# Performance work log

Measured on AMD Instinct MI355X. Metric: run time of the kernel, lower is better.

Reference implementation:

```python
import jax, jax.numpy as jnp
import numpy as np

D = 1024
H = 16
DK = D // H
EPS = 1e-5


def _layernorm(x, g, b):
    mu = jnp.mean(x, axis=-1, keepdims=True)
    var = jnp.var(x, axis=-1, keepdims=True)
    return (x - mu) * jax.lax.rsqrt(var + EPS) * g + b


def setup_inputs() -> dict:
    key = jax.random.key(0)
    ks = jax.random.split(key, 8)
    N, T = 4, 2048
    # module initializes Wqkv/Wout with torch.randn (std=1); mimic that scale
    x = jax.random.normal(ks[0], (N, T, D), dtype=jnp.float32)
    mask = jnp.zeros((N, 1, 1, T), dtype=jnp.float32)  # additive padding mask
    Wqkv = jax.random.normal(ks[1], (D, 3 * D), dtype=jnp.float32)
    Wout = jax.random.normal(ks[2], (D, D), dtype=jnp.float32)
    ln1_g = jnp.ones((D,), jnp.float32); ln1_b = jnp.zeros((D,), jnp.float32)
    ln2_g = jnp.ones((D,), jnp.float32); ln2_b = jnp.zeros((D,), jnp.float32)
    s1 = (1.0 / np.sqrt(D)); s2 = (1.0 / np.sqrt(4 * D))
    W1 = jax.random.uniform(ks[3], (D, 4 * D), jnp.float32, -s1, s1)
    b1 = jnp.zeros((4 * D,), jnp.float32)
    W2 = jax.random.uniform(ks[4], (4 * D, D), jnp.float32, -s2, s2)
    b2 = jnp.zeros((D,), jnp.float32)
    return dict(x=x, mask=mask, Wqkv=Wqkv, Wout=Wout, ln1_g=ln1_g, ln1_b=ln1_b,
                ln2_g=ln2_g, ln2_b=ln2_b, W1=W1, b1=b1, W2=W2, b2=b2)


def reference(x, mask, Wqkv, Wout, ln1_g, ln1_b, ln2_g, ln2_b, W1, b1, W2, b2):
    N, T, _ = x.shape
    # --- attention sublayer: Residual(PreNorm(MHSA)) ---
    z = _layernorm(x, ln1_g, ln1_b)
    qkv = z @ Wqkv  # [N,T,3D]
    Q, K, V = jnp.split(qkv, 3, axis=-1)
    Q, K, V = [a.reshape(N, T, H, DK).swapaxes(1, 2) for a in (Q, K, V)]  # [N,H,T,dk]
    scores = jnp.einsum('nhtd,nhsd->nhts', Q, K) * (DK ** -0.5) + mask
    attn = jax.nn.softmax(scores, axis=-1)  # dropout in eval mode = identity
    ctx = jnp.einsum('nhts,nhsd->nhtd', attn, V)
    attn_out = ctx.swapaxes(1, 2).reshape(N, T, D) @ Wout
    x = x + attn_out
    # --- FFN sublayer: Residual(PreNorm(FFN)), exact (erf) GELU ---
    z = _layernorm(x, ln2_g, ln2_b)
    h = jax.nn.gelu(z @ W1 + b1, approximate=False)
    x = x + (h @ W2 + b2)
    return x
```

## Files before the change

kernel.cpp:

```cpp
#include <hip/hip_runtime.h>
#include <math.h>

#define DEV __device__ __forceinline__

typedef short bf16x8 __attribute__((ext_vector_type(8)));
typedef float f32x4 __attribute__((ext_vector_type(4)));

DEV float bf2f(short s){
  union{ float f; unsigned u; } v; v.u = ((unsigned)(unsigned short)s) << 16; return v.f;
}
DEV short f2b(float f){
  union{ float f; unsigned u; } v; v.f = f;
  unsigned r = v.u + 0x7fffu + ((v.u >> 16) & 1u);
  return (short)(r >> 16);
}
DEV unsigned pk2(float a, float b){
  return ((unsigned)(unsigned short)f2b(b) << 16) | (unsigned short)f2b(a);
}

DEV void gll16(const void* g, void* l){
  __builtin_amdgcn_global_load_lds((const __attribute__((address_space(1))) void*)g,
                                   (__attribute__((address_space(3))) void*)l, 16, 0, 0);
}

template<bool SPLIT>
__global__ void tsplit_kernel(const float* __restrict__ in, short* __restrict__ hi,
                              short* __restrict__ lo, int R, int C){
  __shared__ float tile[32][33];
  int tc = blockIdx.x*32, tr = blockIdx.y*32;
  int lx = threadIdx.x, ly = threadIdx.y;
  for (int i = 0; i < 32; i += 8)
    tile[ly+i][lx] = in[(size_t)(tr+ly+i)*C + tc+lx];
  __syncthreads();
  for (int i = 0; i < 32; i += 8){
    float v = tile[lx][ly+i];
    size_t o = (size_t)(tc+ly+i)*R + tr+lx;
    short h_ = f2b(v); hi[o] = h_;
    if constexpr (SPLIT) lo[o] = f2b(v - bf2f(h_));
  }
}

template<bool SPLIT>
__global__ void ln_kernel(const float* __restrict__ x, const float* __restrict__ g,
                          const float* __restrict__ bta, short* __restrict__ hi,
                          short* __restrict__ lo){
  int row = blockIdx.x, tid = threadIdx.x;
  const float* xr = x + (size_t)row*1024;
  float v[4], s = 0.f, q = 0.f;
  #pragma unroll
  for (int i = 0; i < 4; i++){ v[i] = xr[tid + i*256]; s += v[i]; q += v[i]*v[i]; }
  #pragma unroll
  for (int m = 1; m < 64; m <<= 1){ s += __shfl_xor(s, m); q += __shfl_xor(q, m); }
  __shared__ float red[8];
  int wave = tid >> 6, lane = tid & 63;
  if (lane == 0){ red[wave] = s; red[4+wave] = q; }
  __syncthreads();
  s = red[0]+red[1]+red[2]+red[3];
  q = red[4]+red[5]+red[6]+red[7];
  float mu = s * (1.f/1024.f);
  float var = q * (1.f/1024.f) - mu*mu;
  float rstd = rsqrtf(var + 1e-5f);
  #pragma unroll
  for (int i = 0; i < 4; i++){
    int d = tid + i*256;
    float z = (v[i]-mu)*rstd*g[d] + bta[d];
    short h_ = f2b(z);
    hi[(size_t)row*1024 + d] = h_;
    if constexpr (SPLIT) lo[(size_t)row*1024 + d] = f2b(z - bf2f(h_));
  }
}

constexpr int BM = 128, BN = 128, BK = 32;

template<int MODE, bool SPLIT>
__global__ __launch_bounds__(256, 2) void gemm_kernel(
    const short* __restrict__ Ahi, const short* __restrict__ Alo,
    const short* __restrict__ Bhi, const short* __restrict__ Blo,
    int M, int N, int K,
    float* __restrict__ outf, short* __restrict__ outb,
    const float* __restrict__ res, const float* __restrict__ bias,
    short* __restrict__ qhi, short* __restrict__ qlo,
    short* __restrict__ khi, short* __restrict__ klo,
    short* __restrict__ vbf)
{
  __shared__ short lds[(SPLIT ? 4 : 2) * BM * BK];
  short* sAhi = lds;
  short* sBhi = lds + BM*BK;
  short* sAlo = lds;
  short* sBlo = lds;
  if constexpr (SPLIT){ sAlo = lds + 2*BM*BK; sBlo = lds + 3*BM*BK; }

  const int tid = threadIdx.x;
  const int wave = tid >> 6, lane = tid & 63;
  const int bm = blockIdx.y * BM, bn = blockIdx.x * BN;
  const int wm = (wave >> 1) * 64, wn = (wave & 1) * 64;

  f32x4 acc[4][4] = {};

  const int srow = lane >> 2;
  const int skq  = (lane & 3) * 8;

  for (int k0 = 0; k0 < K; k0 += BK){
    #pragma unroll
    for (int i = 0; i < 2; i++){
      int seg = wave*2 + i;
      int row = seg*16 + srow;
      gll16(Ahi + (size_t)(bm+row)*K + k0 + skq, sAhi + seg*16*BK);
      gll16(Bhi + (size_t)(bn+row)*K + k0 + skq, sBhi + seg*16*BK);
      if constexpr (SPLIT){
        gll16(Alo + (size_t)(bm+row)*K + k0 + skq, sAlo + seg*16*BK);
        gll16(Blo + (size_t)(bn+row)*K + k0 + skq, sBlo + seg*16*BK);
      }
    }
    __syncthreads();
    bf16x8 ah[4], bh[4], al[4], bl[4];
    #pragma unroll
    for (int i = 0; i < 4; i++){
      int ra = (wm + i*16 + (lane & 15)) * BK + (lane >> 4) * 8;
      int rb = (wn + i*16 + (lane & 15)) * BK + (lane >> 4) * 8;
      ah[i] = *(const bf16x8*)&sAhi[ra];
      bh[i] = *(const bf16x8*)&sBhi[rb];
      if constexpr (SPLIT){
        al[i] = *(const bf16x8*)&sAlo[ra];
        bl[i] = *(const bf16x8*)&sBlo[rb];
      }
    }
    __syncthreads();
    #pragma unroll
    for (int i = 0; i < 4; i++)
      #pragma unroll
      for (int j = 0; j < 4; j++){
        acc[i][j] = __builtin_amdgcn_mfma_f32_16x16x32_bf16(ah[i], bh[j], acc[i][j], 0, 0, 0);
        if constexpr (SPLIT){
          acc[i][j] = __builtin_amdgcn_mfma_f32_16x16x32_bf16(ah[i], bl[j], acc[i][j], 0, 0, 0);
          acc[i][j] = __builtin_amdgcn_mfma_f32_16x16x32_bf16(al[i], bh[j], acc[i][j], 0, 0, 0);
        }
      }
  }

  const int row0 = bm + wm + (lane >> 4) * 4;
  const int col0 = bn + wn + (lane & 15);
  #pragma unroll
  for (int i = 0; i < 4; i++)
    #pragma unroll
    for (int j = 0; j < 4; j++){
      int col = col0 + j*16;
      #pragma unroll
      for (int r = 0; r < 4; r++){
        int row = row0 + i*16 + r;
        float v = acc[i][j][r];
        if constexpr (MODE == 1){
          size_t o = (size_t)row*N + col;
          outf[o] = res[o] + v;
        } else if constexpr (MODE == 2){
          float t = v + bias[col];
          t = 0.5f * t * (1.0f + erff(t * 0.70710678118654752f));
          outb[(size_t)row*N + col] = f2b(t);
        } else if constexpr (MODE == 3){
          size_t o = (size_t)row*N + col;
          outf[o] = res[o] + v + bias[col];
        } else {
          int nb = row >> 11, tt = row & 2047;
          if (col < 1024){
            int h = col >> 6, dk = col & 63;
            size_t o = ((size_t)(nb*16 + h)*2048 + tt)*64 + dk;
            float vq = v * 0.125f;
            short h_ = f2b(vq); qhi[o] = h_; qlo[o] = f2b(vq - bf2f(h_));
          } else if (col < 2048){
            int c = col - 1024, h = c >> 6, dk = c & 63;
            size_t o = ((size_t)(nb*16 + h)*2048 + tt)*64 + dk;
            short h_ = f2b(v); khi[o] = h_; klo[o] = f2b(v - bf2f(h_));
          } else {
            int c = col - 2048, h = c >> 6, dk = c & 63;
            vbf[((size_t)(nb*16 + h)*64 + dk)*2048 + tt] = f2b(v);
          }
        }
      }
    }
}

__global__ __launch_bounds__(256, 2) void attn_kernel(
    const short* __restrict__ qhi, const short* __restrict__ qlo,
    const short* __restrict__ khi, const short* __restrict__ klo,
    const short* __restrict__ vt,  const float* __restrict__ mask,
    short* __restrict__ ctx)
{
  __shared__ short sKh[128*64];
  __shared__ short sKl[128*64];
  __shared__ short sQV[64*128];
  __shared__ short sP[4*16*128];
  short* sQh = sQV;
  short* sQl = sQV + 4096;
  short* sV  = sQV;

  const int tid = threadIdx.x, wave = tid >> 6, lane = tid & 63;
  const int qd = lane >> 4, n16 = lane & 15;
  const int nh = blockIdx.y, nb = nh >> 4, h = nh & 15;
  const int q0 = blockIdx.x * 64;
  const size_t qoff = ((size_t)nh*2048 + q0)*64;
  const int sw = n16 & 7;

  {
    int cg = ((lane & 7) ^ (lane >> 3)) * 8;
    int rowl = lane >> 3;
    #pragma unroll
    for (int i = 0; i < 2; i++){
      int seg = wave*2 + i;
      int row = seg*8 + rowl;
      gll16(qhi + qoff + (size_t)row*64 + cg, sQh + seg*512);
      gll16(qlo + qoff + (size_t)row*64 + cg, sQl + seg*512);
    }
  }
  __syncthreads();

  bf16x8 bqh[2], bql[2];
  #pragma unroll
  for (int k2 = 0; k2 < 2; k2++){
    int off = (wave*16 + n16)*64 + (((k2*4 + qd) ^ sw) << 3);
    bqh[k2] = *(const bf16x8*)&sQh[off];
    bql[k2] = *(const bf16x8*)&sQl[off];
  }
  __syncthreads();

  float m_i = -1e30f, l_i = 0.f;
  f32x4 o_[4] = {};
  short* myP = sP + wave*2048;

  for (int kt = 0; kt < 2048; kt += 128){
    const size_t koff = ((size_t)nh*2048 + kt)*64;
    {
      int cg = ((lane & 7) ^ (lane >> 3)) * 8;
      int rowl = lane >> 3;
      #pragma unroll
      for (int i = 0; i < 4; i++){
        int seg = wave*4 + i;
        int row = seg*8 + rowl;
        gll16(khi + koff + (size_t)row*64 + cg, sKh + seg*512);
        gll16(klo + koff + (size_t)row*64 + cg, sKl + seg*512);
      }
      #pragma unroll
      for (int i = 0; i < 4; i++){
        int seg = wave*4 + i;
        int dk = seg*4 + qd;
        int cgv = ((lane & 15) ^ (dk & 7)) * 8;
        gll16(vt + ((size_t)nh*64 + dk)*2048 + kt + cgv, sV + seg*512);
      }
    }
    __syncthreads();

    f32x4 sc[8];
    #pragma unroll
    for (int j = 0; j < 8; j++){
      f32x4 z = {};
      #pragma unroll
      for (int k2 = 0; k2 < 2; k2++){
        int off = (j*16 + n16)*64 + (((k2*4 + qd) ^ sw) << 3);
        bf16x8 akh = *(const bf16x8*)&sKh[off];
        bf16x8 akl = *(const bf16x8*)&sKl[off];
        z = __builtin_amdgcn_mfma_f32_16x16x32_bf16(akh, bqh[k2], z, 0, 0, 0);
        z = __builtin_amdgcn_mfma_f32_16x16x32_bf16(akh, bql[k2], z, 0, 0, 0);
        z = __builtin_amdgcn_mfma_f32_16x16x32_bf16(akl, bqh[k2], z, 0, 0, 0);
      }
      sc[j] = z;
    }

    float mk0 = mask[(size_t)nb*2048 + kt + lane];
    float mk1 = mask[(size_t)nb*2048 + kt + 64 + lane];
    float mloc = -1e30f;
    #pragma unroll
    for (int j = 0; j < 8; j++)
      #pragma unroll
      for (int r = 0; r < 4; r++){
        float ma = __shfl(j < 4 ? mk0 : mk1, (j & 3)*16 + qd*4 + r, 64);
        float s = sc[j][r] + ma;
        sc[j][r] = s;
        mloc = fmaxf(mloc, s);
      }
    mloc = fmaxf(mloc, __shfl_xor(mloc, 16, 64));
    mloc = fmaxf(mloc, __shfl_xor(mloc, 32, 64));
    float mnew = fmaxf(m_i, mloc);
    float alpha = __expf(m_i - mnew);
    m_i = mnew;
    float ps = 0.f;
    #pragma unroll
    for (int j = 0; j < 8; j++)
      #pragma unroll
      for (int r = 0; r < 4; r++){
        float p = __expf(sc[j][r] - mnew);
        sc[j][r] = p;
        ps += p;
      }
    ps += __shfl_xor(ps, 16, 64);
    ps += __shfl_xor(ps, 32, 64);
    l_i = l_i*alpha + ps;
    #pragma unroll
    for (int c = 0; c < 4; c++)
      #pragma unroll
      for (int r = 0; r < 4; r++) o_[c][r] *= alpha;

    #pragma unroll
    for (int b = 0; b < 8; b++){
      uint2 w;
      w.x = pk2(sc[b][0], sc[b][1]);
      w.y = pk2(sc[b][2], sc[b][3]);
      int off = n16*128 + ((((b*2 + (qd >> 1)) ^ sw)) << 3) + (qd & 1)*4;
      *(uint2*)&myP[off] = w;
    }

    #pragma unroll
    for (int kq = 0; kq < 4; kq++){
      bf16x8 bp = *(const bf16x8*)&myP[n16*128 + (((kq*4 + qd) ^ sw) << 3)];
      #pragma unroll
      for (int c = 0; c < 4; c++){
        bf16x8 av = *(const bf16x8*)&sV[(c*16 + n16)*128 + (((kq*4 + qd) ^ sw) << 3)];
        o_[c] = __builtin_amdgcn_mfma_f32_16x16x32_bf16(av, bp, o_[c], 0, 0, 0);
      }
    }
    __syncthreads();
  }

  float linv = 1.0f / l_i;
  int row = q0 + wave*16 + n16;
  size_t base = ((size_t)nb*2048 + row)*1024 + h*64;
  #pragma unroll
  for (int c = 0; c < 4; c++){
    uint2 w;
    w.x = pk2(o_[c][0]*linv, o_[c][1]*linv);
    w.y = pk2(o_[c][2]*linv, o_[c][3]*linv);
    *(uint2*)&ctx[base + c*16 + qd*4] = w;
  }
}

extern "C" void kernel_launch(void* const* d_in, const int* in_sizes, int n_in,
                              void* d_out, int out_size, void* d_ws, size_t ws_size,
                              hipStream_t stream)
{
  (void)in_sizes; (void)n_in; (void)out_size; (void)ws_size;
  const float* x    = (const float*)d_in[0];
  const float* mask = (const float*)d_in[1];
  const float* Wqkv = (const float*)d_in[2];
  const float* Wout = (const float*)d_in[3];
  const float* ln1g = (const float*)d_in[4];
  const float* ln1b = (const float*)d_in[5];
  const float* ln2g = (const float*)d_in[6];
  const float* ln2b = (const float*)d_in[7];
  const float* W1   = (const float*)d_in[8];
  const float* b1   = (const float*)d_in[9];
  const float* W2   = (const float*)d_in[10];
  const float* b2   = (const float*)d_in[11];
  float* out = (float*)d_out;

  const int M = 8192;
  const size_t MB = 1024*1024;
  char* ws = (char*)d_ws;

  short* wqT_h = (short*)(ws + 0*MB);
  short* wqT_l = (short*)(ws + 6*MB);
  short* zhi   = (short*)(ws + 12*MB);
  short* zlo   = (short*)(ws + 28*MB);
  short* qh    = (short*)(ws + 44*MB);
  short* ql    = (short*)(ws + 60*MB);
  short* kh    = (short*)(ws + 76*MB);
  short* kl    = (short*)(ws + 92*MB);
  short* vb    = (short*)(ws + 108*MB);
  short* ctx   = (short*)(ws + 0*MB);
  short* woT   = (short*)(ws + 16*MB);
  float* x2    = (float*)(ws + 64*MB);
  short* z2    = (short*)(ws + 96*MB);
  short* w1T   = (short*)(ws + 112*MB);
  short* w2T   = (short*)(ws + 120*MB);
  short* hbuf  = (short*)(ws + 0*MB);

  dim3 tb(32, 8);

  tsplit_kernel<true ><<<dim3(3072/32, 1024/32), tb, 0, stream>>>(Wqkv, wqT_h, wqT_l, 1024, 3072);
  ln_kernel<true ><<<dim3(M), dim3(256), 0, stream>>>(x, ln1g, ln1b, zhi, zlo);

  gemm_kernel<0, true><<<dim3(3072/128, M/128), dim3(256), 0, stream>>>(
      zhi, zlo, wqT_h, wqT_l, M, 3072, 1024,
      nullptr, nullptr, nullptr, nullptr,
      qh, ql, kh, kl, vb);

  tsplit_kernel<false><<<dim3(1024/32, 1024/32), tb, 0, stream>>>(Wout, woT, nullptr, 1024, 1024);

  attn_kernel<<<dim3(2048/64, 64), dim3(256), 0, stream>>>(qh, ql, kh, kl, vb, mask, ctx);

  tsplit_kernel<false><<<dim3(4096/32, 1024/32), tb, 0, stream>>>(W1, w1T, nullptr, 1024, 4096);
  tsplit_kernel<false><<<dim3(1024/32, 4096/32), tb, 0, stream>>>(W2, w2T, nullptr, 4096, 1024);

  gemm_kernel<1, false><<<dim3(1024/128, M/128), dim3(256), 0, stream>>>(
      ctx, nullptr, woT, nullptr, M, 1024, 1024,
      x2, nullptr, x, nullptr,
      nullptr, nullptr, nullptr, nullptr, nullptr);

  ln_kernel<false><<<dim3(M), dim3(256), 0, stream>>>(x2, ln2g, ln2b, z2, nullptr);

  gemm_kernel<2, false><<<dim3(4096/128, M/128), dim3(256), 0, stream>>>(
      z2, nullptr, w1T, nullptr, M, 4096, 1024,
      nullptr, hbuf, nullptr, b1,
      nullptr, nullptr, nullptr, nullptr, nullptr);

  gemm_kernel<3, false><<<dim3(1024/128, M/128), dim3(256), 0, stream>>>(
      hbuf, nullptr, w2T, nullptr, M, 1024, 4096,
      out, nullptr, x2, b2,
      nullptr, nullptr, nullptr, nullptr, nullptr);
}
```

Baseline: 811.2 us.

## Compute V projection in single bf16 and stream V directly from global in attention

Splits the QKV GEMM so that Q/K still use split-precision (hi/lo) while V is computed by a new single-bf16 GEMM mode, cutting a third of the three-pass MFMA work. The attention kernel drops the V shared-memory staging and reads V fragments straight from global memory. It also frees LDS to raise occupancy to 3 blocks per CU, swaps the grid so blocks sharing a head are adjacent, loads the mask as float4 instead of using shuffles, and replaces round-to-nearest bf16 packing of P with truncation via a byte permute. Risks include uncoalesced or higher-latency global V reads and slightly lower accuracy from truncation and single-precision V.

```diff
diff --git a/kernel.cpp b/kernel.cpp
--- a/kernel.cpp
+++ b/kernel.cpp
@@ -16,6 +16,10 @@
 }
 DEV unsigned pk2(float a, float b){
   return ((unsigned)(unsigned short)f2b(b) << 16) | (unsigned short)f2b(a);
+}
+DEV unsigned pk2t(float a, float b){
+  union{ float f; unsigned u; } ua, ub; ua.f = a; ub.f = b;
+  return __builtin_amdgcn_perm(ub.u, ua.u, 0x07060302);
 }
 
 DEV void gll16(const void* g, void* l){
@@ -159,6 +163,10 @@
         } else if constexpr (MODE == 3){
           size_t o = (size_t)row*N + col;
           outf[o] = res[o] + v + bias[col];
+        } else if constexpr (MODE == 4){
+          int nb = row >> 11, tt = row & 2047;
+          int hh = col >> 6, dk = col & 63;
+          vbf[((size_t)(nb*16 + hh)*64 + dk)*2048 + tt] = f2b(v);
         } else {
           int nb = row >> 11, tt = row & 2047;
           if (col < 1024){
@@ -166,20 +174,17 @@
             size_t o = ((size_t)(nb*16 + h)*2048 + tt)*64 + dk;
             float vq = v * 0.125f;
             short h_ = f2b(vq); qhi[o] = h_; qlo[o] = f2b(vq - bf2f(h_));
-          } else if (col < 2048){
+          } else {
             int c = col - 1024, h = c >> 6, dk = c & 63;
             size_t o = ((size_t)(nb*16 + h)*2048 + tt)*64 + dk;
             short h_ = f2b(v); khi[o] = h_; klo[o] = f2b(v - bf2f(h_));
-          } else {
-            int c = col - 2048, h = c >> 6, dk = c & 63;
-            vbf[((size_t)(nb*16 + h)*64 + dk)*2048 + tt] = f2b(v);
           }
         }
       }
     }
 }
 
-__global__ __launch_bounds__(256, 2) void attn_kernel(
+__global__ __launch_bounds__(256, 3) void attn_kernel(
     const short* __restrict__ qhi, const short* __restrict__ qlo,
     const short* __restrict__ khi, const short* __restrict__ klo,
     const short* __restrict__ vt,  const float* __restrict__ mask,
@@ -187,16 +192,14 @@
 {
   __shared__ short sKh[128*64];
   __shared__ short sKl[128*64];
-  __shared__ short sQV[64*128];
   __shared__ short sP[4*16*128];
-  short* sQh = sQV;
-  short* sQl = sQV + 4096;
-  short* sV  = sQV;
+  short* sQh = sP;
+  short* sQl = sP + 4096;
 
   const int tid = threadIdx.x, wave = tid >> 6, lane = tid & 63;
   const int qd = lane >> 4, n16 = lane & 15;
-  const int nh = blockIdx.y, nb = nh >> 4, h = nh & 15;
-  const int q0 = blockIdx.x * 64;
+  const int nh = blockIdx.x, nb = nh >> 4, h = nh & 15;
+  const int q0 = blockIdx.y * 64;
   const size_t qoff = ((size_t)nh*2048 + q0)*64;
   const int sw = n16 & 7;
 
@@ -220,11 +223,12 @@
     bqh[k2] = *(const bf16x8*)&sQh[off];
     bql[k2] = *(const bf16x8*)&sQl[off];
   }
-  __syncthreads();
 
   float m_i = -1e30f, l_i = 0.f;
   f32x4 o_[4] = {};
   short* myP = sP + wave*2048;
+  const float4* mask4 = (const float4*)(mask + (size_t)nb*2048);
+  const short* vbaseh = vt + ((size_t)nh*64)*2048;
 
   for (int kt = 0; kt < 2048; kt += 128){
     const size_t koff = ((size_t)nh*2048 + kt)*64;
@@ -237,13 +241,6 @@
         int row = seg*8 + rowl;
         gll16(khi + koff + (size_t)row*64 + cg, sKh + seg*512);
         gll16(klo + koff + (size_t)row*64 + cg, sKl + seg*512);
-      }
-      #pragma unroll
-      for (int i = 0; i < 4; i++){
-        int seg = wave*4 + i;
-        int dk = seg*4 + qd;
-        int cgv = ((lane & 15) ^ (dk & 7)) * 8;
-        gll16(vt + ((size_t)nh*64 + dk)*2048 + kt + cgv, sV + seg*512);
       }
     }
     __syncthreads();
@@ -264,18 +261,18 @@
       sc[j] = z;
     }
 
-    float mk0 = mask[(size_t)nb*2048 + kt + lane];
-    float mk1 = mask[(size_t)nb*2048 + kt + 64 + lane];
     float mloc = -1e30f;
     #pragma unroll
-    for (int j = 0; j < 8; j++)
+    for (int j = 0; j < 8; j++){
+      float4 mk = mask4[(kt >> 2) + j*4 + qd];
+      const float* mkp = (const float*)&mk;
       #pragma unroll
       for (int r = 0; r < 4; r++){
-        float ma = __shfl(j < 4 ? mk0 : mk1, (j & 3)*16 + qd*4 + r, 64);
-        float s = sc[j][r] + ma;
+        float s = sc[j][r] + mkp[r];
         sc[j][r] = s;
         mloc = fmaxf(mloc, s);
       }
+    }
     mloc = fmaxf(mloc, __shfl_xor(mloc, 16, 64));
     mloc = fmaxf(mloc, __shfl_xor(mloc, 32, 64));
     float mnew = fmaxf(m_i, mloc);
@@ -301,8 +298,8 @@
     #pragma unroll
     for (int b = 0; b < 8; b++){
       uint2 w;
-      w.x = pk2(sc[b][0], sc[b][1]);
-      w.y = pk2(sc[b][2], sc[b][3]);
+      w.x = pk2t(sc[b][0], sc[b][1]);
+      w.y = pk2t(sc[b][2], sc[b][3]);
       int off = n16*128 + ((((b*2 + (qd >> 1)) ^ sw)) << 3) + (qd & 1)*4;
       *(uint2*)&myP[off] = w;
     }
@@ -312,7 +309,7 @@
       bf16x8 bp = *(const bf16x8*)&myP[n16*128 + (((kq*4 + qd) ^ sw) << 3)];
       #pragma unroll
       for (int c = 0; c < 4; c++){
-        bf16x8 av = *(const bf16x8*)&sV[(c*16 + n16)*128 + (((kq*4 + qd) ^ sw) << 3)];
+        bf16x8 av = *(const bf16x8*)&vbaseh[(size_t)(c*16 + n16)*2048 + kt + kq*32 + qd*8];
         o_[c] = __builtin_amdgcn_mfma_f32_16x16x32_bf16(av, bp, o_[c], 0, 0, 0);
       }
     }
@@ -376,14 +373,19 @@
   tsplit_kernel<true ><<<dim3(3072/32, 1024/32), tb, 0, stream>>>(Wqkv, wqT_h, wqT_l, 1024, 3072);
   ln_kernel<true ><<<dim3(M), dim3(256), 0, stream>>>(x, ln1g, ln1b, zhi, zlo);
 
-  gemm_kernel<0, true><<<dim3(3072/128, M/128), dim3(256), 0, stream>>>(
-      zhi, zlo, wqT_h, wqT_l, M, 3072, 1024,
+  gemm_kernel<0, true><<<dim3(2048/128, M/128), dim3(256), 0, stream>>>(
+      zhi, zlo, wqT_h, wqT_l, M, 2048, 1024,
       nullptr, nullptr, nullptr, nullptr,
-      qh, ql, kh, kl, vb);
+      qh, ql, kh, kl, nullptr);
+
+  gemm_kernel<4, false><<<dim3(1024/128, M/128), dim3(256), 0, stream>>>(
+      zhi, nullptr, wqT_h + (size_t)2048*1024, nullptr, M, 1024, 1024,
+      nullptr, nullptr, nullptr, nullptr,
+      nullptr, nullptr, nullptr, nullptr, vb);
 
   tsplit_kernel<false><<<dim3(1024/32, 1024/32), tb, 0, stream>>>(Wout, woT, nullptr, 1024, 1024);
 
-  attn_kernel<<<dim3(2048/64, 64), dim3(256), 0, stream>>>(qh, ql, kh, kl, vb, mask, ctx);
+  attn_kernel<<<dim3(64, 2048/64), dim3(256), 0, stream>>>(qh, ql, kh, kl, vb, mask, ctx);
 
   tsplit_kernel<false><<<dim3(4096/32, 1024/32), tb, 0, stream>>>(W1, w1T, nullptr, 1024, 4096);
   tsplit_kernel<false><<<dim3(1024/32, 4096/32), tb, 0, stream>>>(W2, w2T, nullptr, 4096, 1024);
```

After: 914.9 us. +12.8%, slower.
